# Performance work log

Measured on AMD Instinct MI355X. Metric: run time of the kernel, lower is better.

The kernel has to match this reference:

```python
import jax, jax.numpy as jnp
import numpy as np

SUB_NO = 20
T_NO = 200
T_DATA = 200000
E_NO = 400
I_NO = 100
N_BASIS = 20
COS_SHIFT = 1.0
COS_SCALE = 5.0


def make_cos_basis():
    # (N_BASIS, T_NO) raised-cosine basis in log time
    i = jnp.arange(N_BASIS, dtype=jnp.float32)[:, None]
    phi = (jnp.pi / 2.0) * i
    x = jnp.arange(T_NO, dtype=jnp.float32)[None, :]
    raw = COS_SCALE * jnp.log(x + COS_SHIFT)
    basis = 0.5 * jnp.cos(raw - phi) + 0.5
    keep = (raw >= phi - jnp.pi) & (raw <= phi + jnp.pi)
    return jnp.where(keep, basis, 0.0)


def grouped_causal_conv(syn, kern_flipped):
    # syn: (T, sub), kern_flipped: (sub, T_NO) already time-reversed -> causal filter
    x = jnp.pad(syn.T, ((0, 0), (T_NO - 1, 0)))[None]          # (1, sub, T+T_NO-1)
    out = jax.lax.conv_general_dilated(
        x, kern_flipped[:, None, :], (1,), 'VALID',
        dimension_numbers=('NCH', 'OIH', 'NCH'),
        feature_group_count=syn.shape[1])
    return out[0].T                                             # (T, sub)


def causal_conv1(z_pad, kern_flipped):
    # z_pad: (L,), kern_flipped: (T_NO,) -> valid conv, length L - T_NO + 1
    out = jax.lax.conv_general_dilated(
        z_pad[None, None, :], kern_flipped[None, None, :], (1,), 'VALID',
        dimension_numbers=('NCH', 'OIH', 'NCH'))
    return out[0, 0]


def setup_inputs() -> dict:
    key = jax.random.key(0)
    ks = jax.random.split(key, 12)
    S_e = (jax.random.uniform(ks[0], (T_DATA, E_NO)) < 0.05).astype(jnp.float32)
    S_i = (jax.random.uniform(ks[1], (T_DATA, I_NO)) < 0.05).astype(jnp.float32)
    Z = (jax.random.uniform(ks[2], (T_DATA,)) < 0.02).astype(jnp.float32)
    # binary-tree dendrite adjacency
    C_den = np.zeros((SUB_NO, SUB_NO), dtype=np.int32)
    for c in range(1, SUB_NO):
        C_den[(c - 1) // 2, c] = 1
    C_den = jnp.asarray(C_den)
    e_asn = np.asarray(jax.random.randint(ks[3], (E_NO,), 0, SUB_NO))
    i_asn = np.asarray(jax.random.randint(ks[4], (I_NO,), 0, SUB_NO))
    C_syn_e = np.zeros((SUB_NO, E_NO), dtype=np.float32); C_syn_e[e_asn, np.arange(E_NO)] = 1.0
    C_syn_i = np.zeros((SUB_NO, I_NO), dtype=np.float32); C_syn_i[i_asn, np.arange(I_NO)] = 1.0
    W_syn_ns = jax.random.uniform(ks[5], (SUB_NO, 2)) * 0.1
    W_syn_ns = W_syn_ns.at[:, 1].multiply(-1.0)
    return {
        'S_e': S_e, 'S_i': S_i, 'Z': Z,
        'C_den': C_den,
        'C_syn_e': jnp.asarray(C_syn_e), 'C_syn_i': jnp.asarray(C_syn_i),
        'W_syn_ns': W_syn_ns,
        'Tau_syn_ns': jnp.ones((SUB_NO, 2)) * 3.0,
        'Delta_syn_ns': jnp.zeros((SUB_NO, 2)),
        'W_syn_s': jax.random.normal(ks[6], (SUB_NO, N_BASIS, 2)) * 0.01,
        'W_sub_ns': jnp.ones(SUB_NO) * 0.1,
        'W_sub_s': jnp.ones(SUB_NO) * 0.1,
        'V_o': jax.random.normal(ks[7], (1,)),
        'Theta_ns': jnp.zeros(SUB_NO),
        'Theta_s': jnp.zeros(SUB_NO),
        'hist_s_weights': jax.random.normal(ks[8], (N_BASIS,)) * 0.01,
        'hist_ns_weights': jax.random.normal(ks[9], (N_BASIS,)) * 0.01,
    }


def reference(S_e, S_i, Z, C_den, C_syn_e, C_syn_i, W_syn_ns, Tau_syn_ns,
              Delta_syn_ns, W_syn_s, W_sub_ns, W_sub_s, V_o, Theta_ns,
              Theta_s, hist_s_weights, hist_ns_weights):
    cos_basis = make_cos_basis()
    # --- spike_convolve ---
    syn_e = S_e @ C_syn_e.T                                     # (T, sub)
    syn_i = S_i @ C_syn_i.T
    t = jnp.arange(T_NO, dtype=jnp.float32)[None, :]
    tau_e = Tau_syn_ns[:, 0:1] ** 2
    tau_i = Tau_syn_ns[:, 1:2] ** 2
    t_e = jnp.maximum(t - Delta_syn_ns[:, 0:1], 0.0) / tau_e
    t_i = jnp.maximum(t - Delta_syn_ns[:, 1:2], 0.0) / tau_i
    e_kern_ns = t_e * jnp.exp(-t_e) * W_syn_ns[:, 0:1] ** 2      # (sub, T_NO)
    i_kern_ns = -t_i * jnp.exp(-t_i) * W_syn_ns[:, 1:2] ** 2
    e_kern_s = (W_syn_s[:, :, 0] ** 2) @ cos_basis               # (sub, T_NO)
    i_kern_s = -(W_syn_s[:, :, 1] ** 2) @ cos_basis
    filt_e_ns = grouped_causal_conv(syn_e, jnp.flip(e_kern_ns, 1))
    filt_i_ns = grouped_causal_conv(syn_i, jnp.flip(i_kern_ns, 1))
    filt_e_s = grouped_causal_conv(syn_e, jnp.flip(e_kern_s, 1))
    filt_i_s = grouped_causal_conv(syn_i, jnp.flip(i_kern_s, 1))
    syn_ns = filt_e_ns + filt_i_ns
    syn_s = filt_e_s + filt_i_s
    # --- spike-history filtering of observed root spikes Z ---
    hist_s_kern = hist_s_weights @ cos_basis                     # (T_NO,)
    hist_ns_kern = hist_ns_weights @ cos_basis
    Z_pad = jnp.pad(Z, (T_NO, 0))                                # (T + T_NO,)
    hist_ns_filt = causal_conv1(Z_pad, jnp.flip(hist_ns_kern))[:-1]  # (T,)
    hist_s_filt = causal_conv1(Z_pad, jnp.flip(hist_s_kern))[:-1]
    # --- leaf-to-root tree recursion (unrolled over SUB_NO static nodes) ---
    C_den_f = C_den.astype(syn_s.dtype)
    w_s2 = W_sub_s ** 2
    w_ns2 = W_sub_ns ** 2
    T_data = S_e.shape[0]
    s_out = jnp.zeros((T_data, SUB_NO), dtype=syn_s.dtype)
    ns_out = jnp.zeros((T_data, SUB_NO), dtype=syn_ns.dtype)
    for idx in range(SUB_NO - 1, 0, -1):
        child_s = s_out @ (C_den_f[idx] * w_s2)                  # (T,) 0 if leaf
        child_ns = ns_out @ (C_den_f[idx] * w_ns2)
        s_out = s_out.at[:, idx].set(jnp.tanh(syn_s[:, idx] + child_s + Theta_s[idx]))
        ns_out = ns_out.at[:, idx].set(jnp.tanh(syn_ns[:, idx] + child_ns + Theta_ns[idx]))
    root_child_s = s_out @ (C_den_f[0] * w_s2)
    root_child_ns = ns_out @ (C_den_f[0] * w_ns2)
    s0 = jax.nn.sigmoid(hist_s_filt + syn_s[:, 0] + root_child_s + Theta_s[0])
    ns0 = jnp.tanh(hist_ns_filt + syn_ns[:, 0] + root_child_ns + Theta_ns[0])
    final_V = ns0 * w_ns2[0] + V_o
    final_Z = s0
    out_filters = jnp.vstack((e_kern_ns, i_kern_ns, e_kern_s, i_kern_s,
                              hist_ns_kern[None, :], hist_s_kern[None, :]))
    return final_V, final_Z, out_filters
```

## Files before the change

### kernel.cpp

```cpp
#include <hip/hip_runtime.h>

#define T_DATA 200000
#define E_NO 400
#define I_NO 100
#define SUB_NO 20
#define N_BASIS 20
#define T_NO 200

typedef unsigned short u16;
typedef unsigned int u32;

#define WS_K4    0
#define WS_HIST2 64000
#define WS_LISTS 65600
#define WS_SYNE  131072
#define WS_SYNI  (WS_SYNE + 8000000)
#define WS_SNS   (WS_SYNI + 8000000)
#define WS_SS    (WS_SNS + 8000000)
#define WS_HF    (WS_SS + 8000000)

__device__ __forceinline__ u16 f2bf(float f) {
    union { float f; u32 u; } v; v.f = f;
    u32 u = v.u;
    u32 lsb = (u >> 16) & 1u;
    u += 0x7fffu + lsb;
    return (u16)(u >> 16);
}
__device__ __forceinline__ float bf2f(u16 b) {
    union { u32 u; float f; } v; v.u = ((u32)b) << 16; return v.f;
}
__device__ __forceinline__ void unpack8(uint4 u, float* x) {
    union { u32 u; float f; } c;
    c.u = u.x << 16;          x[0] = c.f;
    c.u = u.x & 0xffff0000u;  x[1] = c.f;
    c.u = u.y << 16;          x[2] = c.f;
    c.u = u.y & 0xffff0000u;  x[3] = c.f;
    c.u = u.z << 16;          x[4] = c.f;
    c.u = u.z & 0xffff0000u;  x[5] = c.f;
    c.u = u.w << 16;          x[6] = c.f;
    c.u = u.w & 0xffff0000u;  x[7] = c.f;
}
__device__ __forceinline__ float fast_tanh(float x) {
    x = fminf(fmaxf(x, -15.f), 15.f);
    float e = __expf(2.f * x);
    return 1.f - 2.f / (e + 1.f);
}
__device__ __forceinline__ float fast_sigmoid(float x) {
    x = fminf(fmaxf(x, -30.f), 30.f);
    return 1.f / (1.f + __expf(-x));
}

__global__ __launch_bounds__(256) void k_setup(
    const float* __restrict__ Wns, const float* __restrict__ Tau,
    const float* __restrict__ Del, const float* __restrict__ Wsyns,
    const float* __restrict__ HwS, const float* __restrict__ HwNS,
    const float* __restrict__ Cse, const float* __restrict__ Csi,
    float4* __restrict__ k4, float2* __restrict__ hist2,
    int* __restrict__ lists, float* __restrict__ outF)
{
    __shared__ float cb[N_BASIS * T_NO];
    __shared__ int easn[E_NO], iasn[I_NO];
    __shared__ int cnt[2 * SUB_NO], cur[2 * SUB_NO];
    const int tid = threadIdx.x;
    const int b = blockIdx.x;
    const float PI = 3.14159265358979323846f;

    if (b == 21) {
        if (tid < 2 * SUB_NO) cnt[tid] = 0;
        __syncthreads();
        for (int j = tid; j < E_NO; j += 256) {
            int a = 0;
            for (int s = 0; s < SUB_NO; ++s)
                if (Cse[s * E_NO + j] > 0.5f) a = s;
            easn[j] = a;
            atomicAdd(&cnt[a], 1);
        }
        for (int j = tid; j < I_NO; j += 256) {
            int a = 0;
            for (int s = 0; s < SUB_NO; ++s)
                if (Csi[s * I_NO + j] > 0.5f) a = s;
            iasn[j] = a;
            atomicAdd(&cnt[SUB_NO + a], 1);
        }
        __syncthreads();
        if (tid == 0) {
            int aE = 0, aI = 0;
            for (int s = 0; s < SUB_NO; ++s) {
                lists[s] = aE;      cur[s] = aE;           aE += cnt[s];
                lists[21 + s] = aI; cur[SUB_NO + s] = aI;  aI += cnt[SUB_NO + s];
            }
            lists[20] = aE;
            lists[41] = aI;
        }
        __syncthreads();
        for (int j = tid; j < E_NO; j += 256) {
            int p = atomicAdd(&cur[easn[j]], 1);
            lists[42 + p] = j;
        }
        for (int j = tid; j < I_NO; j += 256) {
            int p = atomicAdd(&cur[SUB_NO + iasn[j]], 1);
            lists[442 + p] = j;
        }
        return;
    }

    for (int it = tid; it < N_BASIS * T_NO; it += 256) {
        int bb = it / T_NO, j = it - bb * T_NO;
        float phi = 1.57079632679489662f * (float)bb;
        float raw = 5.0f * logf((float)j + 1.0f);
        float v = 0.f;
        if (raw >= phi - PI && raw <= phi + PI) v = 0.5f * cosf(raw - phi) + 0.5f;
        cb[it] = v;
    }
    __syncthreads();

    if (b < 20) {
        const int s = b;
        if (tid < T_NO) {
            const int j = tid;
            float tau_e = Tau[s * 2 + 0]; tau_e *= tau_e;
            float tau_i = Tau[s * 2 + 1]; tau_i *= tau_i;
            float de = Del[s * 2 + 0], di = Del[s * 2 + 1];
            float we = Wns[s * 2 + 0]; we *= we;
            float wi = Wns[s * 2 + 1]; wi *= wi;
            float te = fmaxf((float)j - de, 0.f) / tau_e;
            float ti = fmaxf((float)j - di, 0.f) / tau_i;
            float eNs = te * expf(-te) * we;
            float iNs = -ti * expf(-ti) * wi;
            float eS = 0.f, iS = 0.f;
            for (int bb = 0; bb < N_BASIS; ++bb) {
                float w0 = Wsyns[(s * N_BASIS + bb) * 2 + 0];
                float w1 = Wsyns[(s * N_BASIS + bb) * 2 + 1];
                float c = cb[bb * T_NO + j];
                eS += w0 * w0 * c;
                iS -= w1 * w1 * c;
            }
            int it = s * T_NO + j;
            k4[it] = make_float4(eNs, iNs, eS, iS);
            outF[it]         = eNs;
            outF[4000 + it]  = iNs;
            outF[8000 + it]  = eS;
            outF[12000 + it] = iS;
        }
    } else {
        if (tid < T_NO) {
            const int j = tid;
            float hn = 0.f, hs = 0.f;
            for (int bb = 0; bb < N_BASIS; ++bb) {
                float c = cb[bb * T_NO + j];
                hn += HwNS[bb] * c;
                hs += HwS[bb] * c;
            }
            hist2[j] = make_float2(hn, hs);
            outF[16000 + j] = hn;
            outF[16200 + j] = hs;
        }
    }
}

__global__ __launch_bounds__(256) void k_spikes(
    const float* __restrict__ Se, const float* __restrict__ Si,
    const int* __restrict__ listsg,
    u16* __restrict__ synEb, u16* __restrict__ synIb)
{
    __shared__ __align__(16) float tE[4][4 * 404];
    __shared__ __align__(16) float tI[4][4 * 104];
    __shared__ int leo[21], lio[21];
    __shared__ u16 lei[E_NO], lii[I_NO];
    const int tid = threadIdx.x;
    const int wv = tid >> 6, lane = tid & 63;
    const int t0 = (blockIdx.x * 4 + wv) * 4;

    if (tid < 21) { leo[tid] = listsg[tid]; lio[tid] = listsg[21 + tid]; }
    for (int k = tid; k < E_NO; k += 256) lei[k] = (u16)listsg[42 + k];
    for (int k = tid; k < I_NO; k += 256) lii[k] = (u16)listsg[442 + k];
    __syncthreads();

    const float4* Se4 = (const float4*)(Se + (size_t)t0 * E_NO);
    const float4* Si4 = (const float4*)(Si + (size_t)t0 * I_NO);
    float4 ve[7];
#pragma unroll
    for (int i = 0; i < 7; ++i) {
        int k = lane + i * 64;
        if (k < 400) ve[i] = Se4[k];
    }
    float4 vi0 = make_float4(0.f, 0.f, 0.f, 0.f);
    float4 vi1 = make_float4(0.f, 0.f, 0.f, 0.f);
    if (lane < 100) vi0 = Si4[lane];
    if (lane + 64 < 100) vi1 = Si4[lane + 64];

#pragma unroll
    for (int i = 0; i < 7; ++i) {
        int k = lane + i * 64;
        if (k < 400) {
            int r = k / 100, c = k - r * 100;
            *(float4*)&tE[wv][r * 404 + c * 4] = ve[i];
        }
    }
    if (lane < 100) {
        int r = lane / 25, c = lane - r * 25;
        *(float4*)&tI[wv][r * 104 + c * 4] = vi0;
    }
    if (lane + 64 < 100) {
        int k = lane + 64;
        int r = k / 25, c = k - r * 25;
        *(float4*)&tI[wv][r * 104 + c * 4] = vi1;
    }
    asm volatile("s_waitcnt lgkmcnt(0)" ::: "memory");

#pragma unroll 1
    for (int p = 0; p < 3; ++p) {
        int task = p * 64 + lane;
        if (task < 80) {
            int s = task >> 2, r = task & 3;
            int k0 = leo[s], k1 = leo[s + 1];
            const float* row = &tE[wv][r * 404];
            float a0 = 0.f, a1 = 0.f, a2 = 0.f, a3 = 0.f;
            int k = k0;
            for (; k + 4 <= k1; k += 4) {
                a0 += row[lei[k]];
                a1 += row[lei[k + 1]];
                a2 += row[lei[k + 2]];
                a3 += row[lei[k + 3]];
            }
            for (; k < k1; ++k) a0 += row[lei[k]];
            synEb[(size_t)s * T_DATA + t0 + r] = f2bf((a0 + a1) + (a2 + a3));
        } else if (task < 160) {
            int tt = task - 80;
            int s = tt >> 2, r = tt & 3;
            const float* row = &tI[wv][r * 104];
            float a = 0.f;
            for (int k = lio[s]; k < lio[s + 1]; ++k) a += row[lii[k]];
            synIb[(size_t)s * T_DATA + t0 + r] = f2bf(a);
        }
    }
}

#define TT 512
#define WROW 712
__global__ __launch_bounds__(256) void k_conv(
    const u16* __restrict__ synEb, const u16* __restrict__ synIb,
    const float* __restrict__ Z,
    const float4* __restrict__ k4g, const float2* __restrict__ hist2g,
    u16* __restrict__ synNSb, u16* __restrict__ synSb,
    float2* __restrict__ hfilt)
{
    __shared__ __align__(16) u16 wE[4 * WROW];
    __shared__ __align__(16) u16 wI[4 * WROW];
    __shared__ __align__(16) float4 k4l[4 * T_NO];
    const int tid = threadIdx.x;
    const int t0 = blockIdx.x * TT;
    const int g  = blockIdx.y;
    const int W0 = t0 - 200;

    if (g < 5) {
        for (int q = tid; q < 712; q += 256) {
            int arr = (q >= 356) ? 1 : 0;
            int qq = q - arr * 356;
            int row = qq / 89, c = qq - row * 89;
            int s = g * 4 + row;
            const u16* src = (arr ? synIb : synEb) + (size_t)s * T_DATA;
            u16* dst = (arr ? wI : wE) + row * WROW + c * 8;
            int gg = W0 + c * 8;
            if (gg >= 0 && gg + 8 <= T_DATA) {
                *(uint4*)dst = *(const uint4*)(src + gg);
            } else {
                for (int e = 0; e < 8; ++e) {
                    int t = gg + e;
                    dst[e] = (t >= 0 && t < T_DATA) ? src[t] : (u16)0;
                }
            }
        }
        for (int q = tid; q < 800; q += 256) {
            int su = q / 200, j = q - su * 200;
            k4l[q] = k4g[(g * 4 + su) * T_NO + j];
        }
    } else {
        for (int q = tid; q < 623; q += 256) {
            if (q < 356) ((uint4*)wI)[q] = make_uint4(0, 0, 0, 0);
            else         ((uint4*)wE)[q - 356 + 89] = make_uint4(0, 0, 0, 0);
        }
        for (int c = tid; c < 89; c += 256) {
            int gg = W0 + c * 8;
            u16 zb[8];
            for (int e = 0; e < 8; ++e) {
                int t = gg + e;
                zb[e] = (t >= 0 && t < T_DATA) ? f2bf(Z[t]) : (u16)0;
            }
            u32 w0 = (u32)zb[0] | ((u32)zb[1] << 16);
            u32 w1 = (u32)zb[2] | ((u32)zb[3] << 16);
            u32 w2 = (u32)zb[4] | ((u32)zb[5] << 16);
            u32 w3 = (u32)zb[6] | ((u32)zb[7] << 16);
            *(uint4*)(wE + c * 8) = make_uint4(w0, w1, w2, w3);
        }
        for (int q = tid; q < 800; q += 256) {
            int su = q / 200, j = q - su * 200;
            float4 v = make_float4(0.f, 0.f, 0.f, 0.f);
            if (su == 0) {
                float2 h = hist2g[j];
                v = make_float4(h.x, 0.f, h.y, 0.f);
            }
            k4l[q] = v;
        }
    }
    __syncthreads();

    const int wv = tid >> 6;
    const int slot = tid & 63;
    const int bT = slot * 8;
    const u16* rowE = wE + wv * WROW;
    const u16* rowI = wI + wv * WROW;

    float aN[8], aS2[8];
#pragma unroll
    for (int m = 0; m < 8; ++m) { aN[m] = 0.f; aS2[m] = 0.f; }

#pragma unroll 1
    for (int jj = 0; jj <= 192; jj += 8) {
        const int p = bT + 192 - jj;
        float xe[16], xi[16];
        uint4 eA = *(const uint4*)(rowE + p);
        uint4 eB = *(const uint4*)(rowE + p + 8);
        uint4 iA = *(const uint4*)(rowI + p);
        uint4 iB = *(const uint4*)(rowI + p + 8);
        unpack8(eA, xe); unpack8(eB, xe + 8);
        unpack8(iA, xi); unpack8(iB, xi + 8);
#pragma unroll
        for (int k = 0; k < 8; ++k) {
            float4 kk = k4l[wv * T_NO + jj + k];
#pragma unroll
            for (int m = 0; m < 8; ++m) {
                float e = xe[m + 8 - k];
                float ii = xi[m + 8 - k];
                aN[m]  = fmaf(e, kk.x, fmaf(ii, kk.y, aN[m]));
                aS2[m] = fmaf(e, kk.z, fmaf(ii, kk.w, aS2[m]));
            }
        }
    }

    if (g < 5) {
        const int s = g * 4 + wv;
        const int t = t0 + bT;
        u32 w0 = (u32)f2bf(aN[0]) | ((u32)f2bf(aN[1]) << 16);
        u32 w1 = (u32)f2bf(aN[2]) | ((u32)f2bf(aN[3]) << 16);
        u32 w2 = (u32)f2bf(aN[4]) | ((u32)f2bf(aN[5]) << 16);
        u32 w3 = (u32)f2bf(aN[6]) | ((u32)f2bf(aN[7]) << 16);
        u32 v0 = (u32)f2bf(aS2[0]) | ((u32)f2bf(aS2[1]) << 16);
        u32 v1 = (u32)f2bf(aS2[2]) | ((u32)f2bf(aS2[3]) << 16);
        u32 v2 = (u32)f2bf(aS2[4]) | ((u32)f2bf(aS2[5]) << 16);
        u32 v3 = (u32)f2bf(aS2[6]) | ((u32)f2bf(aS2[7]) << 16);
        if (t + 8 <= T_DATA) {
            *(uint4*)(synNSb + (size_t)s * T_DATA + t) = make_uint4(w0, w1, w2, w3);
            *(uint4*)(synSb  + (size_t)s * T_DATA + t) = make_uint4(v0, v1, v2, v3);
        } else if (t < T_DATA) {
            for (int m = 0; m < 8 && t + m < T_DATA; ++m) {
                synNSb[(size_t)s * T_DATA + t + m] = f2bf(aN[m]);
                synSb[(size_t)s * T_DATA + t + m] = f2bf(aS2[m]);
            }
        }
    } else if (wv == 0) {
#pragma unroll
        for (int m = 0; m < 8; ++m) {
            int tt = t0 + bT + m + 1;
            if (tt < T_DATA) hfilt[tt] = make_float2(aN[m], aS2[m]);
        }
        if (blockIdx.x == 0 && tid == 0) hfilt[0] = make_float2(0.f, 0.f);
    }
}

#define CT 256
__global__ __launch_bounds__(256) void k_tree(
    const u16* __restrict__ synNSb, const u16* __restrict__ synSb,
    const float2* __restrict__ hfilt,
    const int* __restrict__ Cden,
    const float* __restrict__ WsubNS, const float* __restrict__ WsubS,
    const float* __restrict__ Vo, const float* __restrict__ ThNS,
    const float* __restrict__ ThS,
    float* __restrict__ outV, float* __restrict__ outZ)
{
    __shared__ __align__(16) u16 lNS[SUB_NO * CT];
    __shared__ __align__(16) u16 lS[SUB_NO * CT];
    __shared__ float AS[SUB_NO][SUB_NO], AN[SUB_NO][SUB_NO];
    __shared__ float ths[SUB_NO], thn[SUB_NO];
    __shared__ float wn20s, vos;
    const int tid = threadIdx.x;
    const int t0 = blockIdx.x * CT;

    for (int q = tid; q < 1280; q += 256) {
        int arr = (q >= 640) ? 1 : 0;
        int qq = q - arr * 640;
        int row = qq >> 5, c = qq & 31;
        const u16* src = (arr ? synSb : synNSb) + (size_t)row * T_DATA;
        u16* dst = (arr ? lS : lNS) + row * CT + c * 8;
        int gg = t0 + c * 8;
        if (gg + 8 <= T_DATA) {
            *(uint4*)dst = *(const uint4*)(src + gg);
        } else {
            for (int e = 0; e < 8; ++e) {
                int t = gg + e;
                dst[e] = (t < T_DATA) ? src[t] : (u16)0;
            }
        }
    }
    for (int k = tid; k < SUB_NO * SUB_NO; k += 256) {
        int idx = k / SUB_NO, c = k - idx * SUB_NO;
        float m = (float)Cden[k];
        float wsv = WsubS[c];
        float wnv = WsubNS[c];
        AS[idx][c] = m * wsv * wsv;
        AN[idx][c] = m * wnv * wnv;
    }
    if (tid < SUB_NO) { ths[tid] = ThS[tid]; thn[tid] = ThNS[tid]; }
    if (tid == 0) {
        float w = WsubNS[0];
        wn20s = w * w;
        vos = Vo[0];
    }
    __syncthreads();

    const int t = t0 + tid;
    float2 hf = make_float2(0.f, 0.f);
    if (t < T_DATA) hf = hfilt[t];

    float vs[SUB_NO], vn[SUB_NO];
#pragma unroll
    for (int c = 0; c < SUB_NO; ++c) { vs[c] = 0.f; vn[c] = 0.f; }
#pragma unroll
    for (int idx = SUB_NO - 1; idx >= 1; --idx) {
        float cs = 0.f, cn = 0.f;
#pragma unroll
        for (int c = 0; c < SUB_NO; ++c) {
            cs = fmaf(AS[idx][c], vs[c], cs);
            cn = fmaf(AN[idx][c], vn[c], cn);
        }
        float synS_v = bf2f(lS[idx * CT + tid]);
        float synN_v = bf2f(lNS[idx * CT + tid]);
        vs[idx] = fast_tanh(synS_v + cs + ths[idx]);
        vn[idx] = fast_tanh(synN_v + cn + thn[idx]);
    }
    float cs0 = 0.f, cn0 = 0.f;
#pragma unroll
    for (int c = 0; c < SUB_NO; ++c) {
        cs0 = fmaf(AS[0][c], vs[c], cs0);
        cn0 = fmaf(AN[0][c], vn[c], cn0);
    }
    float s0  = fast_sigmoid(hf.y + bf2f(lS[tid]) + cs0 + ths[0]);
    float ns0 = fast_tanh(hf.x + bf2f(lNS[tid]) + cn0 + thn[0]);

    if (t < T_DATA) {
        outV[t] = ns0 * wn20s + vos;
        outZ[t] = s0;
    }
}

extern "C" void kernel_launch(void* const* d_in, const int* in_sizes, int n_in,
                              void* d_out, int out_size, void* d_ws, size_t ws_size,
                              hipStream_t stream)
{
    const float* Se    = (const float*)d_in[0];
    const float* Si    = (const float*)d_in[1];
    const float* Z     = (const float*)d_in[2];
    const int*   Cden  = (const int*)d_in[3];
    const float* Cse   = (const float*)d_in[4];
    const float* Csi   = (const float*)d_in[5];
    const float* Wns   = (const float*)d_in[6];
    const float* Tau   = (const float*)d_in[7];
    const float* Del   = (const float*)d_in[8];
    const float* Wsyns = (const float*)d_in[9];
    const float* WsubNS= (const float*)d_in[10];
    const float* WsubS = (const float*)d_in[11];
    const float* Vo    = (const float*)d_in[12];
    const float* ThNS  = (const float*)d_in[13];
    const float* ThS   = (const float*)d_in[14];
    const float* HwS   = (const float*)d_in[15];
    const float* HwNS  = (const float*)d_in[16];

    char* ws = (char*)d_ws;
    float4* k4    = (float4*)(ws + WS_K4);
    float2* hist2 = (float2*)(ws + WS_HIST2);
    int*    lists = (int*)(ws + WS_LISTS);
    u16*    synEb = (u16*)(ws + WS_SYNE);
    u16*    synIb = (u16*)(ws + WS_SYNI);
    u16*    synNSb= (u16*)(ws + WS_SNS);
    u16*    synSb = (u16*)(ws + WS_SS);
    float2* hfilt = (float2*)(ws + WS_HF);

    float* outV = (float*)d_out;
    float* outZ = outV + T_DATA;
    float* outF = outV + 2 * T_DATA;

    k_setup<<<22, 256, 0, stream>>>(Wns, Tau, Del, Wsyns, HwS, HwNS, Cse, Csi,
                                    k4, hist2, lists, outF);
    k_spikes<<<T_DATA / 16, 256, 0, stream>>>(Se, Si, lists, synEb, synIb);
    dim3 gc((T_DATA + TT - 1) / TT, 6);
    k_conv<<<gc, 256, 0, stream>>>(synEb, synIb, Z, k4, hist2,
                                   synNSb, synSb, hfilt);
    k_tree<<<(T_DATA + CT - 1) / CT, 256, 0, stream>>>(
        synNSb, synSb, hfilt, Cden, WsubNS, WsubS, Vo, ThNS, ThS,
        outV, outZ);
}
```

Baseline: 630.2 us.

## Replace gather-sum synapse aggregation with ballot bitmasks and popcount

The setup kernel now builds per-subunit 64-bit membership bitmasks instead of index lists. The spike kernel has each wave process 64 time steps, ballots the nonzero spike lanes, and counts per-subunit spikes with popcount against those masks. It then writes results through an LDS tile so the stores are coalesced along time. This relies on the spike inputs being binary 0/1, since the weighted float sum is replaced by a count of nonzero entries.

```diff
diff --git a/kernel.cpp b/kernel.cpp
--- a/kernel.cpp
+++ b/kernel.cpp
@@ -9,10 +9,11 @@
 
 typedef unsigned short u16;
 typedef unsigned int u32;
+typedef unsigned long long u64;
 
 #define WS_K4    0
 #define WS_HIST2 64000
-#define WS_LISTS 65600
+#define WS_MASKS 65600
 #define WS_SYNE  131072
 #define WS_SYNI  (WS_SYNE + 8000000)
 #define WS_SNS   (WS_SYNI + 8000000)
@@ -56,51 +57,35 @@
     const float* __restrict__ HwS, const float* __restrict__ HwNS,
     const float* __restrict__ Cse, const float* __restrict__ Csi,
     float4* __restrict__ k4, float2* __restrict__ hist2,
-    int* __restrict__ lists, float* __restrict__ outF)
+    u32* __restrict__ masks32, float* __restrict__ outF)
 {
     __shared__ float cb[N_BASIS * T_NO];
-    __shared__ int easn[E_NO], iasn[I_NO];
-    __shared__ int cnt[2 * SUB_NO], cur[2 * SUB_NO];
+    __shared__ u32 m32[480];
     const int tid = threadIdx.x;
     const int b = blockIdx.x;
     const float PI = 3.14159265358979323846f;
 
     if (b == 21) {
-        if (tid < 2 * SUB_NO) cnt[tid] = 0;
+        for (int k = tid; k < 480; k += 256) m32[k] = 0;
         __syncthreads();
         for (int j = tid; j < E_NO; j += 256) {
             int a = 0;
             for (int s = 0; s < SUB_NO; ++s)
                 if (Cse[s * E_NO + j] > 0.5f) a = s;
-            easn[j] = a;
-            atomicAdd(&cnt[a], 1);
+            int ch = j >> 8, r = j & 255, ln = r >> 2, cp = r & 3;
+            int widx = (a * 8 + ch * 4 + cp) * 2 + (ln >> 5);
+            atomicOr(&m32[widx], 1u << (ln & 31));
         }
         for (int j = tid; j < I_NO; j += 256) {
             int a = 0;
             for (int s = 0; s < SUB_NO; ++s)
                 if (Csi[s * I_NO + j] > 0.5f) a = s;
-            iasn[j] = a;
-            atomicAdd(&cnt[SUB_NO + a], 1);
+            int ln = j >> 2, cp = j & 3;
+            int widx = 320 + (a * 4 + cp) * 2 + (ln >> 5);
+            atomicOr(&m32[widx], 1u << (ln & 31));
         }
         __syncthreads();
-        if (tid == 0) {
-            int aE = 0, aI = 0;
-            for (int s = 0; s < SUB_NO; ++s) {
-                lists[s] = aE;      cur[s] = aE;           aE += cnt[s];
-                lists[21 + s] = aI; cur[SUB_NO + s] = aI;  aI += cnt[SUB_NO + s];
-            }
-            lists[20] = aE;
-            lists[41] = aI;
-        }
-        __syncthreads();
-        for (int j = tid; j < E_NO; j += 256) {
-            int p = atomicAdd(&cur[easn[j]], 1);
-            lists[42 + p] = j;
-        }
-        for (int j = tid; j < I_NO; j += 256) {
-            int p = atomicAdd(&cur[SUB_NO + iasn[j]], 1);
-            lists[442 + p] = j;
-        }
+        for (int k = tid; k < 480; k += 256) masks32[k] = m32[k];
         return;
     }
 
@@ -160,79 +145,69 @@
 
 __global__ __launch_bounds__(256) void k_spikes(
     const float* __restrict__ Se, const float* __restrict__ Si,
-    const int* __restrict__ listsg,
+    const u64* __restrict__ masks,
     u16* __restrict__ synEb, u16* __restrict__ synIb)
 {
-    __shared__ __align__(16) float tE[4][4 * 404];
-    __shared__ __align__(16) float tI[4][4 * 104];
-    __shared__ int leo[21], lio[21];
-    __shared__ u16 lei[E_NO], lii[I_NO];
+    __shared__ u16 tile[4][40 * 66];
     const int tid = threadIdx.x;
     const int wv = tid >> 6, lane = tid & 63;
-    const int t0 = (blockIdx.x * 4 + wv) * 4;
-
-    if (tid < 21) { leo[tid] = listsg[tid]; lio[tid] = listsg[21 + tid]; }
-    for (int k = tid; k < E_NO; k += 256) lei[k] = (u16)listsg[42 + k];
-    for (int k = tid; k < I_NO; k += 256) lii[k] = (u16)listsg[442 + k];
-    __syncthreads();
-
-    const float4* Se4 = (const float4*)(Se + (size_t)t0 * E_NO);
-    const float4* Si4 = (const float4*)(Si + (size_t)t0 * I_NO);
-    float4 ve[7];
-#pragma unroll
-    for (int i = 0; i < 7; ++i) {
-        int k = lane + i * 64;
-        if (k < 400) ve[i] = Se4[k];
-    }
-    float4 vi0 = make_float4(0.f, 0.f, 0.f, 0.f);
-    float4 vi1 = make_float4(0.f, 0.f, 0.f, 0.f);
-    if (lane < 100) vi0 = Si4[lane];
-    if (lane + 64 < 100) vi1 = Si4[lane + 64];
-
-#pragma unroll
-    for (int i = 0; i < 7; ++i) {
-        int k = lane + i * 64;
-        if (k < 400) {
-            int r = k / 100, c = k - r * 100;
-            *(float4*)&tE[wv][r * 404 + c * 4] = ve[i];
-        }
-    }
-    if (lane < 100) {
-        int r = lane / 25, c = lane - r * 25;
-        *(float4*)&tI[wv][r * 104 + c * 4] = vi0;
-    }
-    if (lane + 64 < 100) {
-        int k = lane + 64;
-        int r = k / 25, c = k - r * 25;
-        *(float4*)&tI[wv][r * 104 + c * 4] = vi1;
+    const int t0 = (blockIdx.x * 4 + wv) * 64;
+    if (t0 >= T_DATA) return;
+
+    u64 me0 = 0, me1 = 0, me2 = 0, me3 = 0, me4 = 0, me5 = 0, me6 = 0, me7 = 0;
+    u64 mi0 = 0, mi1 = 0, mi2 = 0, mi3 = 0;
+    if (lane < 20) {
+        const u64* mp = masks + lane * 8;
+        me0 = mp[0]; me1 = mp[1]; me2 = mp[2]; me3 = mp[3];
+        me4 = mp[4]; me5 = mp[5]; me6 = mp[6]; me7 = mp[7];
+    } else if (lane < 40) {
+        const u64* mp = masks + 160 + (lane - 20) * 4;
+        mi0 = mp[0]; mi1 = mp[1]; mi2 = mp[2]; mi3 = mp[3];
+    }
+    u16* tw = tile[wv];
+
+#pragma unroll 2
+    for (int tt = 0; tt < 64; ++tt) {
+        const int t = t0 + tt;
+        const float4* rE = (const float4*)(Se + (size_t)t * E_NO);
+        const float4* rI = (const float4*)(Si + (size_t)t * I_NO);
+        float4 e0 = rE[lane];
+        float4 e1 = make_float4(0.f, 0.f, 0.f, 0.f);
+        if (lane < 36) e1 = rE[64 + lane];
+        float4 i0 = make_float4(0.f, 0.f, 0.f, 0.f);
+        if (lane < 25) i0 = rI[lane];
+        u64 b0 = __ballot(e0.x != 0.f);
+        u64 b1 = __ballot(e0.y != 0.f);
+        u64 b2 = __ballot(e0.z != 0.f);
+        u64 b3 = __ballot(e0.w != 0.f);
+        u64 b4 = __ballot(e1.x != 0.f);
+        u64 b5 = __ballot(e1.y != 0.f);
+        u64 b6 = __ballot(e1.z != 0.f);
+        u64 b7 = __ballot(e1.w != 0.f);
+        u64 c0 = __ballot(i0.x != 0.f);
+        u64 c1 = __ballot(i0.y != 0.f);
+        u64 c2 = __ballot(i0.z != 0.f);
+        u64 c3 = __ballot(i0.w != 0.f);
+        if (lane < 20) {
+            int c = __popcll(b0 & me0) + __popcll(b1 & me1)
+                  + __popcll(b2 & me2) + __popcll(b3 & me3)
+                  + __popcll(b4 & me4) + __popcll(b5 & me5)
+                  + __popcll(b6 & me6) + __popcll(b7 & me7);
+            tw[lane * 66 + tt] = (u16)c;
+        } else if (lane < 40) {
+            int c = __popcll(c0 & mi0) + __popcll(c1 & mi1)
+                  + __popcll(c2 & mi2) + __popcll(c3 & mi3);
+            tw[lane * 66 + tt] = (u16)c;
+        }
     }
     asm volatile("s_waitcnt lgkmcnt(0)" ::: "memory");
 
-#pragma unroll 1
-    for (int p = 0; p < 3; ++p) {
-        int task = p * 64 + lane;
-        if (task < 80) {
-            int s = task >> 2, r = task & 3;
-            int k0 = leo[s], k1 = leo[s + 1];
-            const float* row = &tE[wv][r * 404];
-            float a0 = 0.f, a1 = 0.f, a2 = 0.f, a3 = 0.f;
-            int k = k0;
-            for (; k + 4 <= k1; k += 4) {
-                a0 += row[lei[k]];
-                a1 += row[lei[k + 1]];
-                a2 += row[lei[k + 2]];
-                a3 += row[lei[k + 3]];
-            }
-            for (; k < k1; ++k) a0 += row[lei[k]];
-            synEb[(size_t)s * T_DATA + t0 + r] = f2bf((a0 + a1) + (a2 + a3));
-        } else if (task < 160) {
-            int tt = task - 80;
-            int s = tt >> 2, r = tt & 3;
-            const float* row = &tI[wv][r * 104];
-            float a = 0.f;
-            for (int k = lio[s]; k < lio[s + 1]; ++k) a += row[lii[k]];
-            synIb[(size_t)s * T_DATA + t0 + r] = f2bf(a);
-        }
+#pragma unroll 4
+    for (int s = 0; s < 40; ++s) {
+        float f = (float)tw[s * 66 + lane];
+        u16 b = f2bf(f);
+        if (s < 20) synEb[(size_t)s * T_DATA + t0 + lane] = b;
+        else        synIb[(size_t)(s - 20) * T_DATA + t0 + lane] = b;
     }
 }
 
@@ -478,7 +453,7 @@
     char* ws = (char*)d_ws;
     float4* k4    = (float4*)(ws + WS_K4);
     float2* hist2 = (float2*)(ws + WS_HIST2);
-    int*    lists = (int*)(ws + WS_LISTS);
+    u64*    masks = (u64*)(ws + WS_MASKS);
     u16*    synEb = (u16*)(ws + WS_SYNE);
     u16*    synIb = (u16*)(ws + WS_SYNI);
     u16*    synNSb= (u16*)(ws + WS_SNS);
@@ -490,8 +465,8 @@
     float* outF = outV + 2 * T_DATA;
 
     k_setup<<<22, 256, 0, stream>>>(Wns, Tau, Del, Wsyns, HwS, HwNS, Cse, Csi,
-                                    k4, hist2, lists, outF);
-    k_spikes<<<T_DATA / 16, 256, 0, stream>>>(Se, Si, lists, synEb, synIb);
+                                    k4, hist2, (u32*)masks, outF);
+    k_spikes<<<(3125 + 3) / 4, 256, 0, stream>>>(Se, Si, masks, synEb, synIb);
     dim3 gc((T_DATA + TT - 1) / TT, 6);
     k_conv<<<gc, 256, 0, stream>>>(synEb, synIb, Z, k4, hist2,
                                    synNSb, synSb, hfilt);
```

Result: no change. 634.1 us (+0.6%).
